# Performance work log

Measured on AMD Instinct MI355X. Metric: run time of the kernel, lower is better.

## Reference

```python
import jax, jax.numpy as jnp
import numpy as np

N_NODES = 100000
N_EDGES = 1600000
D_IN = 64
D_OUT = 64


def setup_inputs() -> dict:
    key = jax.random.key(0)
    k1, k2, k3, k4 = jax.random.split(key, 4)
    features = jax.random.normal(k1, (N_NODES, D_IN), dtype=jnp.float32)
    src = jax.random.randint(k2, (N_EDGES,), 0, N_NODES, dtype=jnp.int32)
    dst = jax.random.randint(k3, (N_EDGES,), 0, N_NODES, dtype=jnp.int32)
    # nn.Linear(input_dim, output_dim): W is [out, in], bias [out]
    W = jax.random.normal(k4, (D_OUT, D_IN), dtype=jnp.float32) * (1.0 / np.sqrt(D_IN))
    b = jnp.zeros((D_OUT,), dtype=jnp.float32)
    return {"features": features, "src": src, "dst": dst, "W": W, "b": b}


def reference(features, src, dst, W, b):
    # DGL update_all(copy_src('h'), sum('m')): for each node v, h[v] = sum over
    # in-edges (u -> v) of features[u].  Gather at src, segment-sum at dst.
    msgs = features[src]  # [E, D_in]
    agg = jax.ops.segment_sum(msgs, dst, num_segments=features.shape[0])  # [N, D_in]
    # nn.Linear: agg @ W.T + b
    return agg @ W.T + b
```

## Files before the change

### kernel.cpp

```cpp
#include <hip/hip_runtime.h>

#define NN 100000
#define NE 1600000
#define D 64
#define BKT_SHIFT 6
#define BKT_NODES 64
#define BKT_MASK 63
#define NBKT 1563
#define SRC_MASK 0x1FFFF
#define EPB 8192
#define NPB ((NE + EPB - 1) / EPB)
#define BINCAP 1280
#define TROWS 16
#define TGRID 2048

__device__ __forceinline__ unsigned short f2bf(float f) {
    unsigned u = __float_as_uint(f);
    unsigned r = u + 0x7FFF + ((u >> 16) & 1);
    return (unsigned short)(r >> 16);
}

__device__ __forceinline__ int cmp4(const int4& v, int k) {
    return k == 0 ? v.x : k == 1 ? v.y : k == 2 ? v.z : v.w;
}

__global__ __launch_bounds__(256) void seed_cursor(int* __restrict__ cursor) {
    const int i = blockIdx.x * 256 + threadIdx.x;
    if (i < NBKT) cursor[i] = 0;
}

__global__ __launch_bounds__(256) void fused_tp2(const float* __restrict__ feat,
                                                 const float* __restrict__ W,
                                                 unsigned short* __restrict__ hb,
                                                 const int* __restrict__ src,
                                                 const int* __restrict__ dst,
                                                 int* __restrict__ cursor,
                                                 int* __restrict__ binned) {
    __shared__ int hist[NBKT];
    __shared__ float4 rowLds[TROWS][16];

    if (blockIdx.x < NPB) {
        for (int i = threadIdx.x; i < NBKT; i += 256) hist[i] = 0;
        __syncthreads();

        const int4* __restrict__ src4 = (const int4*)src;
        const int4* __restrict__ dst4 = (const int4*)dst;
        const int qlo = blockIdx.x * (EPB / 4);
        const int nq  = NE / 4;

        int4 dv[8];
        int  rk[8][4];
#pragma unroll
        for (int it = 0; it < 8; ++it) {
            const int idx = qlo + it * 256 + threadIdx.x;
            dv[it] = (idx < nq) ? dst4[idx] : make_int4(-1, -1, -1, -1);
        }
#pragma unroll
        for (int it = 0; it < 8; ++it)
#pragma unroll
            for (int k = 0; k < 4; ++k) {
                const int d = cmp4(dv[it], k);
                if (d >= 0) rk[it][k] = atomicAdd(&hist[d >> BKT_SHIFT], 1);
            }
        __syncthreads();

        for (int i = threadIdx.x; i < NBKT; i += 256) {
            const int c = hist[i];
            int base = i * BINCAP;
            if (c) base += atomicAdd(&cursor[i], c);
            hist[i] = base;
        }
        __syncthreads();

#pragma unroll
        for (int it = 0; it < 8; ++it) {
            const int idx = qlo + it * 256 + threadIdx.x;
            if (idx < nq) {
                const int4 s4 = src4[idx];
#pragma unroll
                for (int k = 0; k < 4; ++k) {
                    const int d = cmp4(dv[it], k);
                    const int s = cmp4(s4, k);
                    binned[hist[d >> BKT_SHIFT] + rk[it][k]] =
                        s | ((d & BKT_MASK) << 17);
                }
            }
        }
    } else {
        const int bid  = blockIdx.x - NPB;
        const int lane = threadIdx.x & 63;
        const int wv   = threadIdx.x >> 6;
        float4 wreg[16];
        const float4* __restrict__ W4 = (const float4*)W;
#pragma unroll
        for (int i = 0; i < 16; ++i) wreg[i] = W4[lane * 16 + i];

        const int nTiles = NN / TROWS;
        for (int tile = bid; tile < nTiles; tile += TGRID) {
            const int rowBase = tile * TROWS;
            rowLds[threadIdx.x >> 4][threadIdx.x & 15] =
                ((const float4*)(feat + (size_t)(rowBase + (threadIdx.x >> 4)) * D))[threadIdx.x & 15];
            __syncthreads();
            float a0 = 0.f, a1 = 0.f, a2 = 0.f, a3 = 0.f;
#pragma unroll
            for (int k4 = 0; k4 < 16; ++k4) {
                const float4 w  = wreg[k4];
                const float4 r0 = rowLds[wv * 4 + 0][k4];
                const float4 r1 = rowLds[wv * 4 + 1][k4];
                const float4 r2 = rowLds[wv * 4 + 2][k4];
                const float4 r3 = rowLds[wv * 4 + 3][k4];
                a0 += r0.x * w.x + r0.y * w.y + r0.z * w.z + r0.w * w.w;
                a1 += r1.x * w.x + r1.y * w.y + r1.z * w.z + r1.w * w.w;
                a2 += r2.x * w.x + r2.y * w.y + r2.z * w.z + r2.w * w.w;
                a3 += r3.x * w.x + r3.y * w.y + r3.z * w.z + r3.w * w.w;
            }
            const size_t ob = (size_t)(rowBase + wv * 4) * D + lane;
            hb[ob]         = f2bf(a0);
            hb[ob + D]     = f2bf(a1);
            hb[ob + 2 * D] = f2bf(a2);
            hb[ob + 3 * D] = f2bf(a3);
            __syncthreads();
        }
    }
}

__global__ __launch_bounds__(256) void bucket_gather(const uint2* __restrict__ hb2,
                                                     const int* __restrict__ binned,
                                                     const int* __restrict__ cursor,
                                                     const float* __restrict__ bias,
                                                     float4* __restrict__ out4) {
    __shared__ int cnt[BKT_NODES];
    __shared__ int pre[BKT_NODES];
    __shared__ int sEdge[BINCAP];
    const int t = threadIdx.x;
    const int b = blockIdx.x;
    if (t < BKT_NODES) cnt[t] = 0;
    __syncthreads();

    const int gbase = b * BINCAP;
    int sz = cursor[b];
    if (sz > BINCAP) sz = BINCAP;

    int pk[5], dd[5], rr[5];
#pragma unroll
    for (int it = 0; it < 5; ++it) {
        const int e = it * 256 + t;
        if (e < sz) {
            const int p = binned[gbase + e];
            dd[it] = (p >> 17) & BKT_MASK;
            pk[it] = p & SRC_MASK;
            rr[it] = atomicAdd(&cnt[dd[it]], 1);
        } else dd[it] = -1;
    }
    __syncthreads();

    if (t < 64) {
        int v = cnt[t];
#pragma unroll
        for (int s = 1; s < 64; s <<= 1) {
            const int u = __shfl_up(v, s);
            if (t >= s) v += u;
        }
        pre[t] = v;
    }
    __syncthreads();

#pragma unroll
    for (int it = 0; it < 5; ++it) {
        if (dd[it] >= 0)
            sEdge[pre[dd[it]] - cnt[dd[it]] + rr[it]] = pk[it];
    }
    __syncthreads();

    const int q  = t >> 4;
    const int c4 = t & 15;
    const float4 bv = ((const float4*)bias)[c4];
#pragma unroll
    for (int i = 0; i < 4; ++i) {
        const int n    = q * 4 + i;
        const int node = b * BKT_NODES + n;
        if (node >= NN) break;
        const int end = pre[n];
        float ax = 0.f, ay = 0.f, az = 0.f, aw = 0.f;
        for (int e = end - cnt[n]; e < end; e += 8) {
            uint2 x[8];
#pragma unroll
            for (int j = 0; j < 8; ++j) {
                const int idx = (e + j < end) ? sEdge[e + j] : -1;
                x[j] = (idx >= 0) ? hb2[(size_t)idx * 16 + c4] : make_uint2(0u, 0u);
            }
#pragma unroll
            for (int j = 0; j < 8; ++j) {
                ax += __uint_as_float(x[j].x << 16);
                ay += __uint_as_float(x[j].x & 0xFFFF0000u);
                az += __uint_as_float(x[j].y << 16);
                aw += __uint_as_float(x[j].y & 0xFFFF0000u);
            }
        }
        float4 v;
        v.x = ax + bv.x; v.y = ay + bv.y; v.z = az + bv.z; v.w = aw + bv.w;
        out4[(size_t)node * 16 + c4] = v;
    }
}

extern "C" void kernel_launch(void* const* d_in, const int* in_sizes, int n_in,
                              void* d_out, int out_size, void* d_ws, size_t ws_size,
                              hipStream_t stream) {
    const float* feat = (const float*)d_in[0];
    const int*   src  = (const int*)d_in[1];
    const int*   dst  = (const int*)d_in[2];
    const float* W    = (const float*)d_in[3];
    const float* b    = (const float*)d_in[4];
    float* out = (float*)d_out;

    unsigned short* hb = (unsigned short*)d_ws;
    int* binned = (int*)(hb + (size_t)NN * D);
    int* cursor = binned + NBKT * BINCAP;

    seed_cursor<<<(NBKT + 255) / 256, 256, 0, stream>>>(cursor);
    fused_tp2<<<NPB + TGRID, 256, 0, stream>>>(feat, W, hb, src, dst, cursor, binned);
    bucket_gather<<<NBKT, 256, 0, stream>>>((const uint2*)hb, binned, cursor,
                                            b, (float4*)out);
}
```

Measured before the change: 152.0 us.

## Use atomic work-stealing for transform tiles so binning blocks also join in

Replaces the fixed split between binning blocks and transform blocks with a global atomic tile-chunk counter. Every block, including those that finish their edge-binning work, claims chunks of four 16-row tiles until all are done. Edges per binning block are halved, which doubles the number of binning blocks and shortens their per-thread register arrays. The aim is to balance load between the two phases and remove idle tail time, at the cost of extra atomic claims and block-wide barriers per chunk.

Result: slower. 176.3 us (+16.0%).

```diff
diff --git a/kernel.cpp b/kernel.cpp
--- a/kernel.cpp
+++ b/kernel.cpp
@@ -8,10 +8,13 @@
 #define BKT_MASK 63
 #define NBKT 1563
 #define SRC_MASK 0x1FFFF
-#define EPB 8192
+#define EPB 4096
 #define NPB ((NE + EPB - 1) / EPB)
 #define BINCAP 1280
 #define TROWS 16
+#define NTILE (NN / TROWS)
+#define TCHUNK 4
+#define NCHUNKT ((NTILE + TCHUNK - 1) / TCHUNK)
 #define TGRID 2048
 
 __device__ __forceinline__ unsigned short f2bf(float f) {
@@ -26,7 +29,7 @@
 
 __global__ __launch_bounds__(256) void seed_cursor(int* __restrict__ cursor) {
     const int i = blockIdx.x * 256 + threadIdx.x;
-    if (i < NBKT) cursor[i] = 0;
+    if (i < NBKT + 1) cursor[i] = 0;
 }
 
 __global__ __launch_bounds__(256) void fused_tp2(const float* __restrict__ feat,
@@ -38,9 +41,11 @@
                                                  int* __restrict__ binned) {
     __shared__ int hist[NBKT];
     __shared__ float4 rowLds[TROWS][16];
+    __shared__ int claimS;
+    const int t = threadIdx.x;
 
     if (blockIdx.x < NPB) {
-        for (int i = threadIdx.x; i < NBKT; i += 256) hist[i] = 0;
+        for (int i = t; i < NBKT; i += 256) hist[i] = 0;
         __syncthreads();
 
         const int4* __restrict__ src4 = (const int4*)src;
@@ -48,15 +53,15 @@
         const int qlo = blockIdx.x * (EPB / 4);
         const int nq  = NE / 4;
 
-        int4 dv[8];
-        int  rk[8][4];
-#pragma unroll
-        for (int it = 0; it < 8; ++it) {
-            const int idx = qlo + it * 256 + threadIdx.x;
+        int4 dv[4];
+        int  rk[4][4];
+#pragma unroll
+        for (int it = 0; it < 4; ++it) {
+            const int idx = qlo + it * 256 + t;
             dv[it] = (idx < nq) ? dst4[idx] : make_int4(-1, -1, -1, -1);
         }
 #pragma unroll
-        for (int it = 0; it < 8; ++it)
+        for (int it = 0; it < 4; ++it)
 #pragma unroll
             for (int k = 0; k < 4; ++k) {
                 const int d = cmp4(dv[it], k);
@@ -64,7 +69,7 @@
             }
         __syncthreads();
 
-        for (int i = threadIdx.x; i < NBKT; i += 256) {
+        for (int i = t; i < NBKT; i += 256) {
             const int c = hist[i];
             int base = i * BINCAP;
             if (c) base += atomicAdd(&cursor[i], c);
@@ -73,8 +78,8 @@
         __syncthreads();
 
 #pragma unroll
-        for (int it = 0; it < 8; ++it) {
-            const int idx = qlo + it * 256 + threadIdx.x;
+        for (int it = 0; it < 4; ++it) {
+            const int idx = qlo + it * 256 + t;
             if (idx < nq) {
                 const int4 s4 = src4[idx];
 #pragma unroll
@@ -86,40 +91,49 @@
                 }
             }
         }
-    } else {
-        const int bid  = blockIdx.x - NPB;
-        const int lane = threadIdx.x & 63;
-        const int wv   = threadIdx.x >> 6;
+    }
+
+    {
+        const int lane = t & 63;
+        const int wv   = t >> 6;
         float4 wreg[16];
         const float4* __restrict__ W4 = (const float4*)W;
 #pragma unroll
         for (int i = 0; i < 16; ++i) wreg[i] = W4[lane * 16 + i];
-
-        const int nTiles = NN / TROWS;
-        for (int tile = bid; tile < nTiles; tile += TGRID) {
-            const int rowBase = tile * TROWS;
-            rowLds[threadIdx.x >> 4][threadIdx.x & 15] =
-                ((const float4*)(feat + (size_t)(rowBase + (threadIdx.x >> 4)) * D))[threadIdx.x & 15];
+        int* tilectr = cursor + NBKT;
+
+        for (;;) {
             __syncthreads();
-            float a0 = 0.f, a1 = 0.f, a2 = 0.f, a3 = 0.f;
-#pragma unroll
-            for (int k4 = 0; k4 < 16; ++k4) {
-                const float4 w  = wreg[k4];
-                const float4 r0 = rowLds[wv * 4 + 0][k4];
-                const float4 r1 = rowLds[wv * 4 + 1][k4];
-                const float4 r2 = rowLds[wv * 4 + 2][k4];
-                const float4 r3 = rowLds[wv * 4 + 3][k4];
-                a0 += r0.x * w.x + r0.y * w.y + r0.z * w.z + r0.w * w.w;
-                a1 += r1.x * w.x + r1.y * w.y + r1.z * w.z + r1.w * w.w;
-                a2 += r2.x * w.x + r2.y * w.y + r2.z * w.z + r2.w * w.w;
-                a3 += r3.x * w.x + r3.y * w.y + r3.z * w.z + r3.w * w.w;
-            }
-            const size_t ob = (size_t)(rowBase + wv * 4) * D + lane;
-            hb[ob]         = f2bf(a0);
-            hb[ob + D]     = f2bf(a1);
-            hb[ob + 2 * D] = f2bf(a2);
-            hb[ob + 3 * D] = f2bf(a3);
+            if (t == 0) claimS = atomicAdd(tilectr, 1);
             __syncthreads();
+            const int c = claimS;
+            if (c >= NCHUNKT) break;
+            const int tend = min(NTILE, (c + 1) * TCHUNK);
+            for (int tile = c * TCHUNK; tile < tend; ++tile) {
+                const int rowBase = tile * TROWS;
+                rowLds[t >> 4][t & 15] =
+                    ((const float4*)(feat + (size_t)(rowBase + (t >> 4)) * D))[t & 15];
+                __syncthreads();
+                float a0 = 0.f, a1 = 0.f, a2 = 0.f, a3 = 0.f;
+#pragma unroll
+                for (int k4 = 0; k4 < 16; ++k4) {
+                    const float4 w  = wreg[k4];
+                    const float4 r0 = rowLds[wv * 4 + 0][k4];
+                    const float4 r1 = rowLds[wv * 4 + 1][k4];
+                    const float4 r2 = rowLds[wv * 4 + 2][k4];
+                    const float4 r3 = rowLds[wv * 4 + 3][k4];
+                    a0 += r0.x * w.x + r0.y * w.y + r0.z * w.z + r0.w * w.w;
+                    a1 += r1.x * w.x + r1.y * w.y + r1.z * w.z + r1.w * w.w;
+                    a2 += r2.x * w.x + r2.y * w.y + r2.z * w.z + r2.w * w.w;
+                    a3 += r3.x * w.x + r3.y * w.y + r3.z * w.z + r3.w * w.w;
+                }
+                const size_t ob = (size_t)(rowBase + wv * 4) * D + lane;
+                hb[ob]         = f2bf(a0);
+                hb[ob + D]     = f2bf(a1);
+                hb[ob + 2 * D] = f2bf(a2);
+                hb[ob + 3 * D] = f2bf(a3);
+                __syncthreads();
+            }
         }
     }
 }
@@ -210,15 +224,15 @@
     const int*   src  = (const int*)d_in[1];
     const int*   dst  = (const int*)d_in[2];
     const float* W    = (const float*)d_in[3];
-    const float* b    = (const float*)d_in[4];
-    float* out = (float*)d_out;
+    const float* bias = (const float*)d_in[4];
+    float4* out = (float4*)d_out;
 
     unsigned short* hb = (unsigned short*)d_ws;
     int* binned = (int*)(hb + (size_t)NN * D);
     int* cursor = binned + NBKT * BINCAP;
 
-    seed_cursor<<<(NBKT + 255) / 256, 256, 0, stream>>>(cursor);
+    seed_cursor<<<(NBKT + 256) / 256, 256, 0, stream>>>(cursor);
     fused_tp2<<<NPB + TGRID, 256, 0, stream>>>(feat, W, hb, src, dst, cursor, binned);
     bucket_gather<<<NBKT, 256, 0, stream>>>((const uint2*)hb, binned, cursor,
-                                            b, (float4*)out);
-}
+                                            bias, out);
+}
```
